# Kernel optimization log

Measured on AMD Instinct MI355X. Metric: run time of the kernel, lower is better.

## Reference

```python
import jax, jax.numpy as jnp
import numpy as np
import math

N, C, T, V = 8, 256, 120, 25
W = 5          # window_size
PAD = 2        # (W + (W-1)*(dil-1) - 1)//2 with dil=1
H = 8          # num_heads
CO = 256       # out_channels
HD = CO // H   # head channels
EPS = 1e-5


def _bn(x, g, b, m, v):
    # eval-mode BatchNorm2d over channel axis 1; x: (N, C, T, V)
    inv = jax.lax.rsqrt(v + EPS)
    return (x - m[None, :, None, None]) * (inv * g)[None, :, None, None] + b[None, :, None, None]


def _mish(x):
    return x * jnp.tanh(jax.nn.softplus(x))


def setup_inputs() -> dict:
    key = jax.random.key(0)
    ks = jax.random.split(key, 16)
    s_in = 1.0 / math.sqrt(C)
    s_out = 1.0 / math.sqrt(CO)
    return {
        "x": jax.random.normal(ks[0], (N, C, T, V), jnp.float32),
        "w_qkv": jax.random.normal(ks[1], (C, 3 * CO), jnp.float32) * s_in,
        "w_out": jax.random.normal(ks[2], (CO, CO), jnp.float32) * s_out,
        "b_out": jax.random.normal(ks[3], (CO,), jnp.float32) * 0.01,
        "bn1_g": jax.random.normal(ks[4], (CO,), jnp.float32) * 0.1 + 1.0,
        "bn1_b": jax.random.normal(ks[5], (CO,), jnp.float32) * 0.1,
        "ffn_w1": jax.random.normal(ks[6], (CO, CO), jnp.float32) * s_out,
        "ffn_w2": jax.random.normal(ks[7], (CO, CO), jnp.float32) * s_out,
        "ffn_g": jax.random.normal(ks[8], (CO,), jnp.float32) * 0.1 + 1.0,
        "ffn_b": jax.random.normal(ks[9], (CO,), jnp.float32) * 0.1,
        "bn2_g": jax.random.normal(ks[10], (CO,), jnp.float32) * 0.1 + 1.0,
        "bn2_b": jax.random.normal(ks[11], (CO,), jnp.float32) * 0.1,
        "bn1_m": jax.random.normal(ks[12], (CO,), jnp.float32) * 0.1,
        "bn1_v": jax.random.uniform(ks[13], (CO,), jnp.float32, 0.5, 1.5),
        "ffn_m": jax.random.normal(ks[14], (CO,), jnp.float32) * 0.1,
        "ffn_v": jax.random.uniform(ks[15], (CO,), jnp.float32, 0.5, 1.5),
        "bn2_m": jnp.zeros((CO,), jnp.float32),
        "bn2_v": jnp.ones((CO,), jnp.float32),
    }


def reference(x, w_qkv, w_out, b_out, bn1_g, bn1_b, ffn_w1, ffn_w2, ffn_g, ffn_b,
              bn2_g, bn2_b, bn1_m, bn1_v, ffn_m, ffn_v, bn2_m, bn2_v):
    L = W * V
    # --- group_window: unfold over T with kernel (W,1), zero padding PAD ---
    xp = jnp.pad(x, ((0, 0), (0, 0), (PAD, PAD), (0, 0)))
    # (N, C, T, W, V): window element w at time t is frame t + w - PAD
    xw = jnp.stack([xp[:, :, w:w + T, :] for w in range(W)], axis=3)
    xg = xw.transpose(0, 2, 3, 4, 1).reshape(N * T, L, C)  # tokens: (N*T, L, C)

    # --- spatio-temporal attention (full softmax over L, scale 1/sqrt(CO)) ---
    qkv = (xg @ w_qkv).reshape(N * T, L, H, 3, HD)
    q, k, v = qkv[..., 0, :], qkv[..., 1, :], qkv[..., 2, :]  # (NT, L, H, HD)
    scores = jnp.einsum('blhd,bmhd->bhlm', q, k) / math.sqrt(CO)
    attn = jax.nn.softmax(scores, axis=-1)
    out = jnp.einsum('bhlm,bmhd->blhd', attn, v).reshape(N * T, L, CO)
    out = out @ w_out + b_out

    # --- mean over window dim, residual (Identity since C == CO), norm1 ---
    inter = out.reshape(N, T, W, V, CO).transpose(0, 4, 1, 2, 3).mean(axis=3)  # (N, CO, T, V)
    inter = _bn(inter + x, bn1_g, bn1_b, bn1_m, bn1_v)

    # --- FFN: 1x1 conv -> Mish -> BN -> 1x1 conv ---
    h = jnp.einsum('oi,nitv->notv', ffn_w1, inter)
    h = _bn(_mish(h), ffn_g, ffn_b, ffn_m, ffn_v)
    h = jnp.einsum('oi,nitv->notv', ffn_w2, h)

    return _bn(h + inter, bn2_g, bn2_b, bn2_m, bn2_v)
```

## Files before the change

kernel.cpp:

```cpp
#include <hip/hip_runtime.h>
#include <hip/hip_bf16.h>


using bf16  = __bf16;
using bf16x8 = __bf16 __attribute__((ext_vector_type(8)));
using f32x4  = float __attribute__((ext_vector_type(4)));
using f32x16 = float __attribute__((ext_vector_type(16)));
using uint32x4 = unsigned int __attribute__((ext_vector_type(4)));

#define GAS __attribute__((address_space(1)))
#define LAS __attribute__((address_space(3)))

__device__ __forceinline__ void gload_lds16(const void* g, void* l) {
  __builtin_amdgcn_global_load_lds((GAS void*)g, (LAS void*)l, 16, 0, 0);
}

__device__ __forceinline__ unsigned cvt_pk_bf16(float lo, float hi) {
  unsigned r;
  asm("v_cvt_pk_bf16_f32 %0, %1, %2" : "=v"(r) : "v"(lo), "v"(hi));
  return r;
}

__device__ __forceinline__ void pl32_swap(unsigned& a, unsigned& b) {
  asm("v_permlane32_swap_b32 %0, %1" : "+v"(a), "+v"(b));
}

__global__ void k_zero(float* out, int n) {
  int i = blockIdx.x * 256 + threadIdx.x;
  if (i < n) out[i] = 0.f;
}

__global__ void k_prep(const float* __restrict__ x,
                       const float* __restrict__ wqkv, const float* __restrict__ wout,
                       const float* __restrict__ b_out,
                       const float* __restrict__ w1, const float* __restrict__ w2,
                       const float* __restrict__ g1, const float* __restrict__ b1,
                       const float* __restrict__ m1, const float* __restrict__ v1,
                       const float* __restrict__ gf, const float* __restrict__ bff,
                       const float* __restrict__ mf, const float* __restrict__ vf,
                       const float* __restrict__ g2, const float* __restrict__ b2,
                       const float* __restrict__ m2, const float* __restrict__ v2,
                       bf16* __restrict__ Xrow, bf16* __restrict__ WqT,
                       bf16* __restrict__ WoT, bf16* __restrict__ W1c,
                       bf16* __restrict__ W2c, float* __restrict__ pb) {
  __shared__ bf16 T[64 * 72];
  const int b = blockIdx.x, tid = threadIdx.x;
  if (b < 1504) {
    const int bx = b % 47, by = (b / 47) & 3, n = b / 188;
    const int tv0 = bx * 64, c0 = by * 64;
    const int la = tid & 63, sub = tid >> 6;
#pragma unroll 4
    for (int i = 0; i < 16; ++i) {
      int c = c0 + sub + i * 4;
      int tv = tv0 + la;
      float v = (tv < 3000) ? x[(size_t)(n * 256 + c) * 3000 + tv] : 0.f;
      T[(sub + i * 4) * 72 + la] = (bf16)v;
    }
    __syncthreads();
#pragma unroll 4
    for (int i = 0; i < 16; ++i) {
      int tvl = sub + i * 4;
      int tv = tv0 + tvl;
      if (tv < 3000)
        Xrow[(size_t)(n * 3100 + 50 + tv) * 256 + c0 + la] = T[la * 72 + tvl];
    }
  } else if (b < 3041) {
    int idx = (b - 1504) * 256 + tid;
    if (idx < 196608) {
      int c = idx / 768, o = idx % 768;
      WqT[o * 256 + c] = (bf16)wqkv[idx];
    } else if (idx < 262144) {
      int j = idx - 196608;
      int c = j >> 8, o = j & 255;
      WoT[o * 256 + c] = (bf16)wout[j];
    } else if (idx < 327680) {
      int j = idx - 262144;
      W1c[j] = (bf16)w1[j];
    } else if (idx < 393216) {
      int j = idx - 327680;
      W2c[j] = (bf16)w2[j];
    } else if (idx < 393472) {
      int k = idx - 393216;
      float s1 = g1[k] * rsqrtf(v1[k] + 1e-5f);
      pb[k]        = s1;
      pb[256 + k]  = b1[k] - m1[k] * s1;
      float sf = gf[k] * rsqrtf(vf[k] + 1e-5f);
      pb[512 + k]  = sf;
      pb[768 + k]  = bff[k] - mf[k] * sf;
      float s2 = g2[k] * rsqrtf(v2[k] + 1e-5f);
      pb[1024 + k] = s2;
      pb[1280 + k] = b2[k] - m2[k] * s2;
      pb[1536 + k] = b_out[k];
    }
  } else {
    int z = b - 3041;
    int idx16 = z * 256 + tid;
    int e0 = idx16 * 8;
    int pr = e0 >> 8, col = e0 & 255;
    int n = pr / 100, r100 = pr % 100;
    int row = n * 3100 + (r100 < 50 ? r100 : 3000 + r100);
    int4 zz = {};
    *(int4*)&Xrow[(size_t)row * 256 + col] = zz;
  }
}

template <int EPI>
__global__ __launch_bounds__(256, 2) void k_gemm(
    const bf16* __restrict__ A, const bf16* __restrict__ BT,
    bf16* __restrict__ Cout, int ldc, int Mreal,
    const float* __restrict__ pb, const bf16* __restrict__ Res,
    float* __restrict__ Out2) {
  __shared__ __align__(16) char smem[19456];
  bf16* As = (bf16*)smem;
  bf16* Bs = (bf16*)(smem + 8192);
  const int tid = threadIdx.x;
  const int w = tid >> 6, lane = tid & 63, q = lane >> 4, l15 = lane & 15;
  const int m0 = blockIdx.x * 128, n0 = blockIdx.y * 128;
  const int wm = (w >> 1) * 64, wn = (w & 1) * 64;
  const int srow = tid >> 2;
  const int scol = (tid & 3) << 3;
  int ar1 = m0 + srow;        if (ar1 >= Mreal) ar1 = Mreal - 1;
  int ar2 = m0 + srow + 64;   if (ar2 >= Mreal) ar2 = Mreal - 1;
  char* ldsA = (char*)As + w * 1024;
  char* ldsB = (char*)Bs + w * 1024;
  f32x4 acc[4][4] = {};

  for (int ks = 0; ks < 8; ++ks) {
    const bf16* ga1 = A  + (size_t)ar1 * 256 + ks * 32 + scol;
    const bf16* ga2 = A  + (size_t)ar2 * 256 + ks * 32 + scol;
    const bf16* gb  = BT + (size_t)(n0 + srow) * 256 + ks * 32 + scol;
    gload_lds16(ga1, ldsA);
    gload_lds16(ga2, ldsA + 4096);
    gload_lds16(gb,            ldsB);
    gload_lds16(gb + 64 * 256, ldsB + 4096);
    __syncthreads();
    bf16x8 af[4], bfr[4];
#pragma unroll
    for (int i = 0; i < 4; ++i) af[i]  = *(const bf16x8*)&As[(wm + i * 16 + l15) * 32 + q * 8];
#pragma unroll
    for (int i = 0; i < 4; ++i) bfr[i] = *(const bf16x8*)&Bs[(wn + i * 16 + l15) * 32 + q * 8];
#pragma unroll
    for (int i = 0; i < 4; ++i)
#pragma unroll
      for (int j = 0; j < 4; ++j)
        acc[i][j] = __builtin_amdgcn_mfma_f32_16x16x32_bf16(af[i], bfr[j], acc[i][j], 0, 0, 0);
    __syncthreads();
  }

  if constexpr (EPI != 3) {
#pragma unroll
    for (int i = 0; i < 4; ++i) {
#pragma unroll
      for (int j = 0; j < 4; ++j) {
#pragma unroll
        for (int r = 0; r < 4; ++r) {
          int row = m0 + wm + i * 16 + q * 4 + r;
          int col = n0 + wn + j * 16 + l15;
          if (row >= Mreal) continue;
          float v = acc[i][j][r];
          if constexpr (EPI == 0) {
            Cout[(size_t)row * ldc + col] = (bf16)v;
          } else if constexpr (EPI == 1) {
            v += pb[1536 + col];
            int n = row / 3000;
            v += (float)Res[(size_t)(row + n * 100 + 50) * 256 + col];
            v = v * pb[col] + pb[256 + col];
            Cout[(size_t)row * 256 + col] = (bf16)v;
          } else {
            float ex = __expf(v);
            float a = 1.f + ex;
            float u = 1.f / (a * a);
            v = v * (1.f - u) / (1.f + u);
            v = v * pb[512 + col] + pb[768 + col];
            Cout[(size_t)row * 256 + col] = (bf16)v;
          }
        }
      }
    }
  } else {
    float* Tt = (float*)smem;
    const int tti = (w & 1);
#pragma unroll
    for (int jj = 0; jj < 4; ++jj) {
      __syncthreads();
#pragma unroll
      for (int i = 0; i < 4; ++i) {
#pragma unroll
        for (int r = 0; r < 4; ++r) {
          int rowl = wm + i * 16 + q * 4 + r;
          int row = m0 + rowl;
          int col = n0 + tti * 64 + jj * 16 + l15;
          float v = acc[i][jj][r];
          v += (float)Res[(size_t)row * 256 + col];
          v = v * pb[1024 + col] + pb[1280 + col];
          Tt[tti * 2432 + rowl * 19 + l15] = v;
        }
      }
      __syncthreads();
#pragma unroll
      for (int k = 0; k < 16; ++k) {
        int flat = k * 256 + tid;
        int tt2 = flat >> 11;
        int rem = flat & 2047;
        int colL = rem >> 7;
        int rowl = rem & 127;
        int row = m0 + rowl;
        if (row < Mreal) {
          int col = n0 + tt2 * 64 + jj * 16 + colL;
          int n = row / 3000, r2 = row - n * 3000;
          Out2[(size_t)(n * 256 + col) * 3000 + r2] = Tt[tt2 * 2432 + rowl * 19 + colL];
        }
      }
    }
  }
}

__global__ __launch_bounds__(256, 4) void k_attn(const bf16* __restrict__ Y,
                                                 bf16* __restrict__ om) {
  __shared__ __align__(16) char smem[18432];
  bf16* Vts = (bf16*)smem;
  float* Ofl = (float*)smem;
  const int tid = threadIdx.x;
  const int bi = blockIdx.x;
  const int h = bi & 7, b = bi >> 3;
  const int n = b / 120, t = b % 120;
  const bf16* Yb = Y + (size_t)(n * 3100 + t * 25) * 768 + h * 96;
  const int w = tid >> 6, lane = tid & 63;
  const int l31 = lane & 31, hi = lane >> 5;

#pragma unroll
  for (int p = 0; p < 2; ++p) {
    int m = p * 64 + lane;
    if (m < 125) {
      int4 v4 = *(const int4*)(Yb + (size_t)m * 768 + 64 + w * 8);
      bf16x8 v8 = __builtin_bit_cast(bf16x8, v4);
#pragma unroll
      for (int jj = 0; jj < 8; ++jj) Vts[(w * 8 + jj) * 136 + m] = v8[jj];
    }
  }
  if (tid < 96) {
    int d = tid / 3, m = 125 + tid % 3;
    Vts[d * 136 + m] = (bf16)0.f;
  }

  int qrow = w * 32 + l31; if (qrow > 124) qrow = 124;
  const bf16* qp = Yb + (size_t)qrow * 768 + hi * 8;
  bf16x8 qf0 = *(const bf16x8*)qp;
  bf16x8 qf1 = *(const bf16x8*)(qp + 16);

  f32x16 acc[4] = {};
#pragma unroll
  for (int kt = 0; kt < 4; ++kt) {
    int krow = kt * 32 + l31; if (krow > 124) krow = 124;
    const bf16* kp = Yb + (size_t)krow * 768 + 32 + hi * 8;
    bf16x8 kf0 = *(const bf16x8*)kp;
    bf16x8 kf1 = *(const bf16x8*)(kp + 16);
    acc[kt] = __builtin_amdgcn_mfma_f32_32x32x16_bf16(kf0, qf0, acc[kt], 0, 0, 0);
    acc[kt] = __builtin_amdgcn_mfma_f32_32x32x16_bf16(kf1, qf1, acc[kt], 0, 0, 0);
  }

  const float lscale = 0.0901387929f;
  float s = 0.f;
#pragma unroll
  for (int kt = 0; kt < 4; ++kt) {
#pragma unroll
    for (int r = 0; r < 16; ++r) {
      float pz = exp2f(acc[kt][r] * lscale);
      if (kt == 3 && r >= 13 && hi) pz = 0.f;
      acc[kt][r] = pz;
      s += pz;
    }
  }
  s += __shfl_xor(s, 32, 64);
  float rinv = 1.f / s;

  __syncthreads();

  f32x16 oacc = {};
#pragma unroll
  for (int kc = 0; kc < 8; ++kc) {
    const int kt = kc >> 1, base = (kc & 1) * 8;
    unsigned a0 = cvt_pk_bf16(acc[kt][base + 0] * rinv, acc[kt][base + 1] * rinv);
    unsigned a1 = cvt_pk_bf16(acc[kt][base + 2] * rinv, acc[kt][base + 3] * rinv);
    unsigned b0 = cvt_pk_bf16(acc[kt][base + 4] * rinv, acc[kt][base + 5] * rinv);
    unsigned b1 = cvt_pk_bf16(acc[kt][base + 6] * rinv, acc[kt][base + 7] * rinv);
    pl32_swap(a0, b0);
    pl32_swap(a1, b1);
    uint32x4 pwv = {a0, a1, b0, b1};
    bf16x8 pa = __builtin_bit_cast(bf16x8, pwv);
    bf16x8 vf = *(const bf16x8*)&Vts[l31 * 136 + kc * 16 + hi * 8];
    oacc = __builtin_amdgcn_mfma_f32_32x32x16_bf16(pa, vf, oacc, 0, 0, 0);
  }

  __syncthreads();
#pragma unroll
  for (int r = 0; r < 16; ++r) {
    int row = w * 32 + (r & 3) + 8 * (r >> 2) + 4 * hi;
    Ofl[row * 36 + l31] = oacc[r];
  }
  __syncthreads();
  bf16* dst = om + (size_t)((n * 120 + t) * 25) * 256 + h * 32;
  for (int j = tid; j < 800; j += 256) {
    int vv = j >> 5, d = j & 31;
    float s5 = 0.f;
#pragma unroll
    for (int ww = 0; ww < 5; ++ww) s5 += Ofl[(ww * 25 + vv) * 36 + d];
    dst[vv * 256 + d] = (bf16)(s5 * 0.2f);
  }
}

extern "C" void kernel_launch(void* const* d_in, const int* in_sizes, int n_in,
                              void* d_out, int out_size, void* d_ws, size_t ws_size,
                              hipStream_t stream) {
  const size_t NEED = 51584000;
  if (ws_size < NEED) {
    k_zero<<<(out_size + 255) / 256, 256, 0, stream>>>((float*)d_out, out_size);
    return;
  }
  const float* x     = (const float*)d_in[0];
  const float* wqkv  = (const float*)d_in[1];
  const float* wout  = (const float*)d_in[2];
  const float* b_out = (const float*)d_in[3];
  const float* bn1_g = (const float*)d_in[4];
  const float* bn1_b = (const float*)d_in[5];
  const float* ffn_w1= (const float*)d_in[6];
  const float* ffn_w2= (const float*)d_in[7];
  const float* ffn_g = (const float*)d_in[8];
  const float* ffn_b = (const float*)d_in[9];
  const float* bn2_g = (const float*)d_in[10];
  const float* bn2_b = (const float*)d_in[11];
  const float* bn1_m = (const float*)d_in[12];
  const float* bn1_v = (const float*)d_in[13];
  const float* ffn_m = (const float*)d_in[14];
  const float* ffn_v = (const float*)d_in[15];
  const float* bn2_m = (const float*)d_in[16];
  const float* bn2_v = (const float*)d_in[17];

  char* ws = (char*)d_ws;
  float* pb    = (float*)(ws + 0);
  bf16* WqT    = (bf16*)(ws + 7168);
  bf16* WoT    = (bf16*)(ws + 400384);
  bf16* W1c    = (bf16*)(ws + 531456);
  bf16* W2c    = (bf16*)(ws + 662528);
  bf16* Xrow   = (bf16*)(ws + 793600);
  bf16* Y      = (bf16*)(ws + 13491200);
  bf16* interR = Y;
  bf16* Gm     = (bf16*)(ws + 25779200);
  bf16* om     = (bf16*)d_out;

  k_prep<<<3141, 256, 0, stream>>>(x, wqkv, wout, b_out, ffn_w1, ffn_w2,
                                   bn1_g, bn1_b, bn1_m, bn1_v,
                                   ffn_g, ffn_b, ffn_m, ffn_v,
                                   bn2_g, bn2_b, bn2_m, bn2_v,
                                   Xrow, WqT, WoT, W1c, W2c, pb);
  k_gemm<0><<<dim3(194, 6), 256, 0, stream>>>(Xrow, WqT, Y, 768, 24800, pb, nullptr, nullptr);
  k_attn<<<7680, 256, 0, stream>>>(Y, om);
  k_gemm<1><<<dim3(188, 2), 256, 0, stream>>>(om, WoT, interR, 256, 24000, pb, Xrow, nullptr);
  k_gemm<2><<<dim3(188, 2), 256, 0, stream>>>(interR, W1c, Gm, 256, 24000, pb, nullptr, nullptr);
  k_gemm<3><<<dim3(188, 2), 256, 0, stream>>>(Gm, W2c, nullptr, 256, 24000, pb, interR, (float*)d_out);
}
```

Before: 244.6 us.

## Fold softmax scale into Q weights and defer normalization to epilogue

The softmax log2 scale is folded into the Q columns of the bf16 QKV weight during preprocessing, so the attention kernel no longer multiplies each score. The 1/sum normalization is moved out of the P·V loop: unnormalized probabilities are packed to bf16 right after exp, and the per-row reciprocal is stored in shared memory and applied in the window-mean epilogue. The PV MFMA chain is also split into two accumulators to shorten the dependency chain. This removes per-element multiplies and repacking work from the critical path, at the cost of bf16 rounding of unnormalized values, extra shared memory and more registers.

```diff
diff --git a/kernel.cpp b/kernel.cpp
--- a/kernel.cpp
+++ b/kernel.cpp
@@ -68,7 +68,9 @@
     int idx = (b - 1504) * 256 + tid;
     if (idx < 196608) {
       int c = idx / 768, o = idx % 768;
-      WqT[o * 256 + c] = (bf16)wqkv[idx];
+      float vv = wqkv[idx];
+      if ((o % 96) < 32) vv *= 0.0901387929f;
+      WqT[o * 256 + c] = (bf16)vv;
     } else if (idx < 262144) {
       int j = idx - 196608;
       int c = j >> 8, o = j & 255;
@@ -217,9 +219,10 @@
 
 __global__ __launch_bounds__(256, 4) void k_attn(const bf16* __restrict__ Y,
                                                  bf16* __restrict__ om) {
-  __shared__ __align__(16) char smem[18432];
+  __shared__ __align__(16) char smem[18944];
   bf16* Vts = (bf16*)smem;
   float* Ofl = (float*)smem;
+  float* Rin = (float*)(smem + 18432);
   const int tid = threadIdx.x;
   const int bi = blockIdx.x;
   const int h = bi & 7, b = bi >> 3;
@@ -259,44 +262,58 @@
     acc[kt] = __builtin_amdgcn_mfma_f32_32x32x16_bf16(kf1, qf1, acc[kt], 0, 0, 0);
   }
 
-  const float lscale = 0.0901387929f;
-  float s = 0.f;
+  float sp[4];
+  uint32x4 pk[8];
 #pragma unroll
   for (int kt = 0; kt < 4; ++kt) {
+    float e[16];
 #pragma unroll
     for (int r = 0; r < 16; ++r) {
-      float pz = exp2f(acc[kt][r] * lscale);
+      float pz = exp2f(acc[kt][r]);
       if (kt == 3 && r >= 13 && hi) pz = 0.f;
-      acc[kt][r] = pz;
-      s += pz;
-    }
-  }
+      e[r] = pz;
+    }
+    float t0 = (e[0] + e[1]) + (e[2] + e[3]);
+    float t1 = (e[4] + e[5]) + (e[6] + e[7]);
+    float t2 = (e[8] + e[9]) + (e[10] + e[11]);
+    float t3 = (e[12] + e[13]) + (e[14] + e[15]);
+    sp[kt] = (t0 + t1) + (t2 + t3);
+#pragma unroll
+    for (int half = 0; half < 2; ++half) {
+      const int ba = half * 8;
+      unsigned a0 = cvt_pk_bf16(e[ba + 0], e[ba + 1]);
+      unsigned a1 = cvt_pk_bf16(e[ba + 2], e[ba + 3]);
+      unsigned b0 = cvt_pk_bf16(e[ba + 4], e[ba + 5]);
+      unsigned b1 = cvt_pk_bf16(e[ba + 6], e[ba + 7]);
+      pl32_swap(a0, b0);
+      pl32_swap(a1, b1);
+      pk[kt * 2 + half][0] = a0;
+      pk[kt * 2 + half][1] = a1;
+      pk[kt * 2 + half][2] = b0;
+      pk[kt * 2 + half][3] = b1;
+    }
+  }
+  float s = (sp[0] + sp[1]) + (sp[2] + sp[3]);
   s += __shfl_xor(s, 32, 64);
   float rinv = 1.f / s;
+  if (hi == 0) Rin[w * 32 + l31] = rinv;
 
   __syncthreads();
 
-  f32x16 oacc = {};
+  f32x16 oacc0 = {}, oacc1 = {};
 #pragma unroll
   for (int kc = 0; kc < 8; ++kc) {
-    const int kt = kc >> 1, base = (kc & 1) * 8;
-    unsigned a0 = cvt_pk_bf16(acc[kt][base + 0] * rinv, acc[kt][base + 1] * rinv);
-    unsigned a1 = cvt_pk_bf16(acc[kt][base + 2] * rinv, acc[kt][base + 3] * rinv);
-    unsigned b0 = cvt_pk_bf16(acc[kt][base + 4] * rinv, acc[kt][base + 5] * rinv);
-    unsigned b1 = cvt_pk_bf16(acc[kt][base + 6] * rinv, acc[kt][base + 7] * rinv);
-    pl32_swap(a0, b0);
-    pl32_swap(a1, b1);
-    uint32x4 pwv = {a0, a1, b0, b1};
-    bf16x8 pa = __builtin_bit_cast(bf16x8, pwv);
+    bf16x8 pa = __builtin_bit_cast(bf16x8, pk[kc]);
     bf16x8 vf = *(const bf16x8*)&Vts[l31 * 136 + kc * 16 + hi * 8];
-    oacc = __builtin_amdgcn_mfma_f32_32x32x16_bf16(pa, vf, oacc, 0, 0, 0);
+    if (kc & 1) oacc1 = __builtin_amdgcn_mfma_f32_32x32x16_bf16(pa, vf, oacc1, 0, 0, 0);
+    else        oacc0 = __builtin_amdgcn_mfma_f32_32x32x16_bf16(pa, vf, oacc0, 0, 0, 0);
   }
 
   __syncthreads();
 #pragma unroll
   for (int r = 0; r < 16; ++r) {
     int row = w * 32 + (r & 3) + 8 * (r >> 2) + 4 * hi;
-    Ofl[row * 36 + l31] = oacc[r];
+    Ofl[row * 36 + l31] = oacc0[r] + oacc1[r];
   }
   __syncthreads();
   bf16* dst = om + (size_t)((n * 120 + t) * 25) * 256 + h * 32;
@@ -304,7 +321,8 @@
     int vv = j >> 5, d = j & 31;
     float s5 = 0.f;
 #pragma unroll
-    for (int ww = 0; ww < 5; ++ww) s5 += Ofl[(ww * 25 + vv) * 36 + d];
+    for (int ww = 0; ww < 5; ++ww)
+      s5 += Ofl[(ww * 25 + vv) * 36 + d] * Rin[ww * 25 + vv];
     dst[vv * 256 + d] = (bf16)(s5 * 0.2f);
   }
 }
```

Result: no change. 245.2 us (+0.3%).
